# Kernel optimization log

Hardware: AMD Instinct MI355X
Metric: run time of the kernel (lower is better)

Reference implementation:

```python
import jax, jax.numpy as jnp
import numpy as np

N = 50000   # nodes
E = 800000  # edges per relation (avg degree 16)
IN = 128    # input feature dim
H = 2       # attention heads per layer
OUT = 64    # output feats per head
R = 2       # number of relations
NEG_SLOPE = 0.2


def _edge_softmax(e, dst, n):
    # e: [E, H] edge scores; softmax over incoming edges of each dst node
    m = jax.ops.segment_max(e, dst, num_segments=n)  # [N, H]
    m = jnp.where(jnp.isfinite(m), m, 0.0)
    ex = jnp.exp(e - jax.lax.stop_gradient(m)[dst])
    s = jax.ops.segment_sum(ex, dst, num_segments=n)  # [N, H]
    return ex / s[dst]


def _gat_layer(h, W, al, ar, b, src, dst):
    # h: [N, in]; W: [R, in, H*OUT]; al/ar: [R, H, OUT]; b: [R, H*OUT]
    # src/dst: [R, E] int32. HeteroGraphConv with sum aggregation over relations.
    acc = jnp.zeros((N, H, OUT), h.dtype)
    for r in range(R):  # small fixed relation count
        f = (h @ W[r]).reshape(N, H, OUT)           # projected feats
        el = (f * al[r]).sum(-1)                    # [N, H]
        er = (f * ar[r]).sum(-1)                    # [N, H]
        e = jax.nn.leaky_relu(el[src[r]] + er[dst[r]], NEG_SLOPE)  # [E, H]
        a = _edge_softmax(e, dst[r], N)             # [E, H]
        msg = f[src[r]] * a[:, :, None]             # [E, H, OUT]
        agg = jax.ops.segment_sum(msg, dst[r], num_segments=N)     # [N, H, OUT]
        acc = acc + jax.nn.elu(agg + b[r].reshape(1, H, OUT))
    return acc.reshape(N, H * OUT)  # flatten(1)


def setup_inputs() -> dict:
    key = jax.random.key(0)
    k = jax.random.split(key, 13)
    s = 0.05
    f32 = jnp.float32
    return {
        "x": jax.random.normal(k[0], (N, IN), f32),
        "W0": jax.random.normal(k[1], (R, IN, H * OUT), f32) * s,
        "al0": jax.random.normal(k[2], (R, H, OUT), f32) * s,
        "ar0": jax.random.normal(k[3], (R, H, OUT), f32) * s,
        "b0": jax.random.normal(k[4], (R, H * OUT), f32) * s,
        "W1": jax.random.normal(k[5], (R, H * OUT, H * OUT), f32) * s,
        "al1": jax.random.normal(k[6], (R, H, OUT), f32) * s,
        "ar1": jax.random.normal(k[7], (R, H, OUT), f32) * s,
        "b1": jax.random.normal(k[8], (R, H * OUT), f32) * s,
        "src0": jax.random.randint(k[9], (R, E), 0, N, jnp.int32),
        "dst0": jax.random.randint(k[10], (R, E), 0, N, jnp.int32),
        "src1": jax.random.randint(k[11], (R, E), 0, N, jnp.int32),
        "dst1": jax.random.randint(k[12], (R, E), 0, N, jnp.int32),
    }


def reference(x, W0, al0, ar0, b0, W1, al1, ar1, b1, src0, dst0, src1, dst1):
    h = _gat_layer(x, W0, al0, ar0, b0, src0, dst0)  # [N, H*OUT]
    h = _gat_layer(h, W1, al1, ar1, b1, src1, dst1)  # [N, H*OUT]
    return h
```

## Files before the change

### kernel.cpp

```cpp
#include <hip/hip_runtime.h>

#define NN 50000
#define NE 800000
#define DIM 128
#define NB 128
#define CH 4096
#define CAP 8192
#define MAXDEG 64
#define BPSET ((NE + CH - 1) / CH)
#define NBIN_BLOCKS (4 * BPSET)

typedef unsigned int uint;
typedef unsigned short ushort;
typedef __attribute__((ext_vector_type(8))) short v8s;
typedef __attribute__((ext_vector_type(4))) float v4f;

__device__ __forceinline__ ushort f2bf(float f) {
    union { float f; uint i; } c; c.f = f;
    const uint r = (c.i + 0x7fffu + ((c.i >> 16) & 1u)) >> 16;
    return (ushort)r;
}

__device__ __forceinline__ void conv_body(
    const float* __restrict__ W0, const float* __restrict__ W1,
    ushort* __restrict__ WT, int bid)
{
    const int t = bid * 256 + threadIdx.x;
#pragma unroll
    for (int i = 0; i < 4; i++) {
        const int o = t * 4 + i;
        const int m = o >> 14, rem = o & 16383;
        const int nrow = rem >> 7, k = rem & 127;
        const float* src = (m < 2) ? (W0 + (size_t)m * 16384)
                                   : (W1 + (size_t)(m - 2) * 16384);
        WT[o] = f2bf(src[k * 128 + nrow]);
    }
}

__device__ __forceinline__ void gemm_body(
    ushort (*tile)[136],
    const ushort* __restrict__ hbf, const float* __restrict__ xf,
    const ushort* __restrict__ WT,
    const float* __restrict__ al, const float* __restrict__ ar,
    ushort* __restrict__ fg0, ushort* __restrict__ fg1,
    float* __restrict__ elb, int n, int is_f32, int bid)
{
    const int tid = threadIdx.x;
    const int w = tid >> 6, lane = tid & 63;
    const int quad = lane >> 4, l16 = lane & 15;
    const int row0 = bid * 64 + w * 16;

    int arow = row0 + l16;
    if (arow >= n) arow = n - 1;

    v8s afr[4];
    if (is_f32) {
        const float* ap = xf + (size_t)arow * DIM + quad * 8;
#pragma unroll
        for (int kt = 0; kt < 4; kt++) {
            const float4 a0 = *(const float4*)(ap + kt * 32);
            const float4 a1 = *(const float4*)(ap + kt * 32 + 4);
            ushort tmp[8] = { f2bf(a0.x), f2bf(a0.y), f2bf(a0.z), f2bf(a0.w),
                              f2bf(a1.x), f2bf(a1.y), f2bf(a1.z), f2bf(a1.w) };
            afr[kt] = *(const v8s*)tmp;
        }
    } else {
        const ushort* ap = hbf + (size_t)arow * DIM + quad * 8;
#pragma unroll
        for (int kt = 0; kt < 4; kt++) afr[kt] = *(const v8s*)(ap + kt * 32);
    }

    for (int rel = 0; rel < 2; rel++) {
        const ushort* bp = WT + (size_t)rel * DIM * DIM + (size_t)l16 * DIM + quad * 8;
        v4f acc[8];
#pragma unroll
        for (int nt = 0; nt < 8; nt++) acc[nt] = (v4f)0.0f;
#pragma unroll
        for (int kt = 0; kt < 4; kt++) {
#pragma unroll
            for (int nt = 0; nt < 8; nt++) {
                const v8s b = *(const v8s*)(bp + (size_t)nt * 16 * DIM + kt * 32);
                acc[nt] = __builtin_amdgcn_mfma_f32_16x16x32_bf16(afr[kt], b, acc[nt], 0, 0, 0);
            }
        }

        const float* alr = al + rel * DIM;
        const float* arr = ar + rel * DIM;
        float pel[4][2], per2[4][2];
#pragma unroll
        for (int r = 0; r < 4; r++)
            pel[r][0] = pel[r][1] = per2[r][0] = per2[r][1] = 0.f;
#pragma unroll
        for (int nt = 0; nt < 8; nt++) {
            const int col = nt * 16 + l16;
            const float av = alr[col], rv = arr[col];
            const int head = nt >> 2;
#pragma unroll
            for (int r = 0; r < 4; r++) {
                pel[r][head] += acc[nt][r] * av;
                per2[r][head] += acc[nt][r] * rv;
            }
        }
#pragma unroll
        for (int o = 1; o < 16; o <<= 1) {
#pragma unroll
            for (int r = 0; r < 4; r++) {
#pragma unroll
                for (int h = 0; h < 2; h++) {
                    pel[r][h] += __shfl_xor(pel[r][h], o);
                    per2[r][h] += __shfl_xor(per2[r][h], o);
                }
            }
        }
        float* elp = elb + (size_t)rel * NN * 4;
        float* erp = elp + (size_t)NN * 2;
        if (l16 == 0) {
#pragma unroll
            for (int r = 0; r < 4; r++) {
                const int row = row0 + quad * 4 + r;
                if (row < n) {
#pragma unroll
                    for (int h = 0; h < 2; h++) {
                        elp[row * 2 + h] = pel[r][h];
                        erp[row * 2 + h] = per2[r][h];
                    }
                }
            }
        }

        __syncthreads();
        const int lr0 = w * 16 + quad * 4;
#pragma unroll
        for (int nt = 0; nt < 8; nt++) {
            const int col = nt * 16 + l16;
#pragma unroll
            for (int r = 0; r < 4; r++)
                tile[lr0 + r][col] = f2bf(acc[nt][r]);
        }
        __syncthreads();
        ushort* fgr = rel ? fg1 : fg0;
        const int srow = tid >> 2, ch = tid & 3;
        const int grow = bid * 64 + srow;
        if (grow < n) {
            const uint4* lp = (const uint4*)&tile[srow][ch * 32];
            uint4* gp = (uint4*)(fgr + (size_t)grow * DIM + ch * 32);
            gp[0] = lp[0];
            gp[1] = lp[1];
            gp[2] = lp[2];
            gp[3] = lp[3];
        }
    }
}

__global__ __launch_bounds__(256) void gemm_dual(
    const ushort* __restrict__ hbf, const float* __restrict__ xf,
    const ushort* __restrict__ WT,
    const float* __restrict__ al, const float* __restrict__ ar,
    ushort* __restrict__ fg0, ushort* __restrict__ fg1,
    float* __restrict__ elb, int n, int is_f32)
{
    __shared__ ushort tile[64][136];
    gemm_body(tile, hbf, xf, WT, al, ar, fg0, fg1, elb, n, is_f32, blockIdx.x);
}

__device__ __forceinline__ void bin_body(
    char* smem,
    const int* __restrict__ dst0, const int* __restrict__ dst1,
    const int* __restrict__ src0, const int* __restrict__ src1,
    int* __restrict__ gcur, uint* __restrict__ binned, int bid)
{
    int* hist  = (int*)smem;
    int* ebase = hist + NB;
    int* lcur  = ebase + NB;
    int* gbase = lcur + NB;
    int* sc    = gbase + NB;
    uint* stage = (uint*)(sc + NB);

    const int s = bid / BPSET, cb = bid - s * BPSET;
    const int* dstp = (s < 2) ? (dst0 + (size_t)s * NE) : (dst1 + (size_t)(s - 2) * NE);
    const int* srcp = (s < 2) ? (src0 + (size_t)s * NE) : (src1 + (size_t)(s - 2) * NE);
    const int e0 = cb * CH;
    const int t = threadIdx.x;

    if (t < NB) hist[t] = 0;
    __syncthreads();

    int myd[16], mys[16];
#pragma unroll
    for (int k = 0; k < 16; k++) {
        const int e = e0 + t + k * 256;
        if (e < NE) {
            const int d = dstp[e];
            myd[k] = d;
            mys[k] = srcp[e];
            atomicAdd(&hist[(d * NB) / NN], 1);
        } else myd[k] = -1;
    }
    __syncthreads();
    if (t < NB) sc[t] = hist[t];
    __syncthreads();
    for (int o = 1; o < NB; o <<= 1) {
        int tv = 0;
        if (t < NB && t >= o) tv = sc[t - o];
        __syncthreads();
        if (t < NB) sc[t] += tv;
        __syncthreads();
    }
    if (t < NB) {
        ebase[t] = sc[t] - hist[t];
        lcur[t]  = sc[t] - hist[t];
        gbase[t] = (s * NB + t) * CAP + atomicAdd(&gcur[s * NB + t], hist[t]);
    }
    __syncthreads();
#pragma unroll
    for (int k = 0; k < 16; k++) {
        if (myd[k] >= 0) {
            const int b = (myd[k] * NB) / NN;
            const int p = atomicAdd(&lcur[b], 1);
            stage[p] = ((uint)myd[k] << 16) | (uint)mys[k];
        }
    }
    __syncthreads();
    const int total = ebase[NB - 1] + hist[NB - 1];
    for (int i = t; i < total; i += 256) {
        const uint v = stage[i];
        const int b = ((int)(v >> 16) * NB) / NN;
        binned[gbase[b] + (i - ebase[b])] = v;
    }
}

__global__ __launch_bounds__(256) void prep_a(
    const float* __restrict__ W0, const float* __restrict__ W1,
    ushort* __restrict__ WT,
    const int* __restrict__ dst0, const int* __restrict__ dst1,
    const int* __restrict__ src0, const int* __restrict__ src1,
    int* __restrict__ gcur, uint* __restrict__ binned)
{
    __shared__ __align__(16) char smem[18944];
    const int bid = blockIdx.x;
    if (bid < 64) {
        conv_body(W0, W1, WT, bid);
    } else {
        bin_body(smem, dst0, dst1, src0, src1, gcur, binned, bid - 64);
    }
}

__device__ __forceinline__ void slot_body(
    int* lcur, const int* __restrict__ gcur, const uint* __restrict__ binned,
    int* __restrict__ cnt, ushort* __restrict__ slots, int bid)
{
    const int s = bid >> 7, b = bid & (NB - 1);
    const int nb0 = (b * NN + NB - 1) / NB;
    int nb1 = ((b + 1) * NN + NB - 1) / NB;
    if (nb1 > NN) nb1 = NN;
    const int nloc = nb1 - nb0;
    int fill = gcur[s * NB + b];
    if (fill > CAP) fill = CAP;
    const uint* bslot = binned + (size_t)(s * NB + b) * CAP;
    const int t = threadIdx.x;

    for (int i = t; i < nloc; i += 256) lcur[i] = 0;
    __syncthreads();
    ushort* sbase = slots + (size_t)s * NN * MAXDEG;
    for (int j = t; j < fill; j += 256) {
        const uint v = bslot[j];
        const int d = (int)(v >> 16);
        const int p = atomicAdd(&lcur[d - nb0], 1);
        if (p < MAXDEG) sbase[(size_t)d * MAXDEG + p] = (ushort)(v & 0xffffu);
    }
    __syncthreads();
    for (int i = t; i < nloc; i += 256) {
        const int c = lcur[i];
        cnt[s * NN + nb0 + i] = c < MAXDEG ? c : MAXDEG;
    }
}

__global__ __launch_bounds__(256) void prep_b(
    const float* __restrict__ xf, const ushort* __restrict__ WT,
    const float* __restrict__ al, const float* __restrict__ ar,
    ushort* __restrict__ fg0, ushort* __restrict__ fg1,
    float* __restrict__ elb,
    const int* __restrict__ gcur, const uint* __restrict__ binned,
    int* __restrict__ cnt, ushort* __restrict__ slots, int gblocks)
{
    __shared__ __align__(16) char smem[17408];
    const int bid = blockIdx.x;
    if (bid < gblocks) {
        gemm_body((ushort(*)[136])smem, nullptr, xf, WT, al, ar,
                  fg0, fg1, elb, NN, 1, bid);
    } else {
        slot_body((int*)smem, gcur, binned, cnt, slots, bid - gblocks);
    }
}

__device__ __forceinline__ float elu(float v) { return v > 0.f ? v : expm1f(v); }
__device__ __forceinline__ float2 bfpair(uint u) {
    union { uint i; float f; } lo, hi;
    lo.i = u << 16;
    hi.i = u & 0xffff0000u;
    return make_float2(lo.f, hi.f);
}

__global__ __launch_bounds__(256) void aggregate_dual(
    const int* __restrict__ cnt0, const ushort* __restrict__ sl0,
    const int* __restrict__ cnt1, const ushort* __restrict__ sl1,
    const float2* __restrict__ el0, const float2* __restrict__ er0,
    const float2* __restrict__ el1, const float2* __restrict__ er1,
    const ushort* __restrict__ fg0, const ushort* __restrict__ fg1,
    const float* __restrict__ bias0, const float* __restrict__ bias1,
    float* __restrict__ outf, ushort* __restrict__ outbf, int obf)
{
    __shared__ uint soff[4][64];
    __shared__ float wts[4][2][64];
    const int wv = (blockIdx.x * 256 + threadIdx.x) >> 6;
    if (wv >= NN) return;
    const int lane = threadIdx.x & 63;
    const int wid = threadIdx.x >> 6;

    const int* cnts[2] = {cnt0, cnt1};
    const ushort* sls[2] = {sl0, sl1};
    const float2* els[2] = {el0, el1};
    const float2* ers[2] = {er0, er1};
    const ushort* fgs[2] = {fg0, fg1};
    const float* biases[2] = {bias0, bias1};

    float oacc0 = 0.f, oacc1 = 0.f;

#pragma unroll
    for (int rel = 0; rel < 2; rel++) {
        int deg = cnts[rel][wv];
        if (deg > MAXDEG) deg = MAXDEG;
        const float2 erd = ers[rel][wv];
        float2 acc = make_float2(0.f, 0.f);

        uint sof = 0;
        float ex0 = 0.f, ex1 = 0.f;
        if (lane < deg) {
            const int s = sls[rel][(size_t)wv * MAXDEG + lane];
            const float2 e = els[rel][s];
            float e0 = e.x + erd.x, e1 = e.y + erd.y;
            e0 = e0 > 0.f ? e0 : 0.2f * e0;
            e1 = e1 > 0.f ? e1 : 0.2f * e1;
            ex0 = __expf(e0);
            ex1 = __expf(e1);
            sof = (uint)s << 8;
        }
        float den0 = ex0, den1 = ex1;
        for (int o = 32; o > 0; o >>= 1) {
            den0 += __shfl_xor(den0, o);
            den1 += __shfl_xor(den1, o);
        }
        const float inv0 = 1.0f / den0, inv1 = 1.0f / den1;
        soff[wid][lane] = sof;
        wts[wid][0][lane] = ex0 * inv0;
        wts[wid][1][lane] = ex1 * inv1;
        const char* fgb = (const char*)fgs[rel] + lane * 4;
        const float* wrow = wts[wid][lane >> 5];
        const uint* sorow = soff[wid];
        const int dp = (deg + 15) & ~15;
        for (int tt = 0; tt < dp; tt += 16) {
            uint off[16];
            float wgt[16];
#pragma unroll
            for (int k = 0; k < 16; k++) {
                off[k] = sorow[tt + k];
                wgt[k] = wrow[tt + k];
            }
            uint u[16];
#pragma unroll
            for (int k = 0; k < 16; k++)
                u[k] = *(const uint*)(fgb + off[k]);
#pragma unroll
            for (int k = 0; k < 16; k++) {
                const float2 f = bfpair(u[k]);
                acc.x += f.x * wgt[k];
                acc.y += f.y * wgt[k];
            }
        }

        const float b0 = biases[rel][2 * lane], b1 = biases[rel][2 * lane + 1];
        oacc0 += elu(acc.x + b0);
        oacc1 += elu(acc.y + b1);
    }

    if (obf) {
        ushort tmp[2] = { f2bf(oacc0), f2bf(oacc1) };
        *(uint*)(outbf + (size_t)wv * DIM + 2 * lane) = *(const uint*)tmp;
    } else {
        float* op = outf + (size_t)wv * DIM + 2 * lane;
        op[0] = oacc0; op[1] = oacc1;
    }
}

extern "C" void kernel_launch(void* const* d_in, const int* in_sizes, int n_in,
                              void* d_out, int out_size, void* d_ws, size_t ws_size,
                              hipStream_t stream)
{
    const float* x   = (const float*)d_in[0];
    const float* W0  = (const float*)d_in[1];
    const float* al0 = (const float*)d_in[2];
    const float* ar0 = (const float*)d_in[3];
    const float* b0  = (const float*)d_in[4];
    const float* W1  = (const float*)d_in[5];
    const float* al1 = (const float*)d_in[6];
    const float* ar1 = (const float*)d_in[7];
    const float* b1  = (const float*)d_in[8];
    const int* src0 = (const int*)d_in[9];
    const int* dst0 = (const int*)d_in[10];
    const int* src1 = (const int*)d_in[11];
    const int* dst1 = (const int*)d_in[12];
    float* out = (float*)d_out;

    char* w = (char*)d_ws;
    auto alloc = [&](size_t bytes) {
        char* p = w; w += (bytes + 255) & ~(size_t)255; return p;
    };
    ushort* h1bf   = (ushort*)alloc((size_t)NN * DIM * 2);
    ushort* fg0    = (ushort*)alloc((size_t)NN * DIM * 2);
    ushort* fg1    = (ushort*)alloc((size_t)NN * DIM * 2);
    ushort* WT     = (ushort*)alloc((size_t)4 * DIM * DIM * 2);
    float*  elb    = (float*)alloc((size_t)8 * NN * 4);
    int*    cnt    = (int*)alloc((size_t)4 * NN * 4);
    ushort* slots  = (ushort*)alloc((size_t)4 * NN * MAXDEG * 2);
    uint*   binned = (uint*)alloc((size_t)4 * NB * CAP * 4);
    int*    gcur   = (int*)alloc((size_t)4 * NB * 4);

    const int gblocks = (NN + 63) / 64;

    hipMemsetAsync(gcur, 0, (size_t)4 * NB * 4, stream);
    prep_a<<<64 + NBIN_BLOCKS, 256, 0, stream>>>(
        W0, W1, WT, dst0, dst1, src0, src1, gcur, binned);
    prep_b<<<gblocks + 4 * NB, 256, 0, stream>>>(
        x, WT, al0, ar0, fg0, fg1, elb, gcur, binned, cnt, slots, gblocks);

    for (int L = 0; L < 2; L++) {
        if (L) {
            gemm_dual<<<gblocks, 256, 0, stream>>>(
                h1bf, nullptr, WT + (size_t)2 * DIM * DIM, al1, ar1,
                fg0, fg1, elb, NN, 0);
        }
        const float* b = L ? b1 : b0;
        const int es0 = L * 2, es1 = L * 2 + 1;
        float* el0p = elb;
        float* er0p = elb + (size_t)NN * 2;
        float* el1p = elb + (size_t)NN * 4;
        float* er1p = elb + (size_t)NN * 6;
        aggregate_dual<<<(NN * 64 + 255) / 256, 256, 0, stream>>>(
            cnt + (size_t)es0 * NN, slots + (size_t)es0 * NN * MAXDEG,
            cnt + (size_t)es1 * NN, slots + (size_t)es1 * NN * MAXDEG,
            (const float2*)el0p, (const float2*)er0p,
            (const float2*)el1p, (const float2*)er1p,
            fg0, fg1, b, b + DIM,
            L ? out : nullptr, L ? nullptr : h1bf, L ? 0 : 1);
    }
}
```

Before: 346.1 us.

## Stage slot lists in shared memory and split fused prep kernel

The slot-building step now scatters edge sources into a shared-memory window per destination bin and then writes the whole window to global memory with coalesced 16-byte stores. Previously each edge did a scattered 2-byte global write. The layer-0 GEMM is no longer fused with slot building in one launch and now runs as its own gemm_dual launch, which adds a kernel launch. The large shared array (about 50KB) limits occupancy of slot_build. The aggregate kernel also drops its redundant degree clamp.

```diff
diff --git a/kernel.cpp b/kernel.cpp
--- a/kernel.cpp
+++ b/kernel.cpp
@@ -7,6 +7,7 @@
 #define CH 4096
 #define CAP 8192
 #define MAXDEG 64
+#define WINMAX 391
 #define BPSET ((NE + CH - 1) / CH)
 #define NBIN_BLOCKS (4 * BPSET)
 
@@ -37,18 +38,18 @@
     }
 }
 
-__device__ __forceinline__ void gemm_body(
-    ushort (*tile)[136],
+__global__ __launch_bounds__(256) void gemm_dual(
     const ushort* __restrict__ hbf, const float* __restrict__ xf,
     const ushort* __restrict__ WT,
     const float* __restrict__ al, const float* __restrict__ ar,
     ushort* __restrict__ fg0, ushort* __restrict__ fg1,
-    float* __restrict__ elb, int n, int is_f32, int bid)
-{
+    float* __restrict__ elb, int n, int is_f32)
+{
+    __shared__ ushort tile[64][136];
     const int tid = threadIdx.x;
     const int w = tid >> 6, lane = tid & 63;
     const int quad = lane >> 4, l16 = lane & 15;
-    const int row0 = bid * 64 + w * 16;
+    const int row0 = blockIdx.x * 64 + w * 16;
 
     int arow = row0 + l16;
     if (arow >= n) arow = n - 1;
@@ -140,7 +141,7 @@
         __syncthreads();
         ushort* fgr = rel ? fg1 : fg0;
         const int srow = tid >> 2, ch = tid & 3;
-        const int grow = bid * 64 + srow;
+        const int grow = blockIdx.x * 64 + srow;
         if (grow < n) {
             const uint4* lp = (const uint4*)&tile[srow][ch * 32];
             uint4* gp = (uint4*)(fgr + (size_t)grow * DIM + ch * 32);
@@ -150,17 +151,6 @@
             gp[3] = lp[3];
         }
     }
-}
-
-__global__ __launch_bounds__(256) void gemm_dual(
-    const ushort* __restrict__ hbf, const float* __restrict__ xf,
-    const ushort* __restrict__ WT,
-    const float* __restrict__ al, const float* __restrict__ ar,
-    ushort* __restrict__ fg0, ushort* __restrict__ fg1,
-    float* __restrict__ elb, int n, int is_f32)
-{
-    __shared__ ushort tile[64][136];
-    gemm_body(tile, hbf, xf, WT, al, ar, fg0, fg1, elb, n, is_f32, blockIdx.x);
 }
 
 __device__ __forceinline__ void bin_body(
@@ -245,10 +235,13 @@
     }
 }
 
-__device__ __forceinline__ void slot_body(
-    int* lcur, const int* __restrict__ gcur, const uint* __restrict__ binned,
-    int* __restrict__ cnt, ushort* __restrict__ slots, int bid)
-{
+__global__ __launch_bounds__(256) void slot_build(
+    const int* __restrict__ gcur, const uint* __restrict__ binned,
+    int* __restrict__ cnt, ushort* __restrict__ slots)
+{
+    __shared__ ushort win[WINMAX * MAXDEG];
+    __shared__ int lcur[WINMAX];
+    const int bid = blockIdx.x;
     const int s = bid >> 7, b = bid & (NB - 1);
     const int nb0 = (b * NN + NB - 1) / NB;
     int nb1 = ((b + 1) * NN + NB - 1) / NB;
@@ -259,37 +252,24 @@
     const uint* bslot = binned + (size_t)(s * NB + b) * CAP;
     const int t = threadIdx.x;
 
+    uint* wz = (uint*)win;
+    for (int i = t; i < WINMAX * MAXDEG / 2; i += 256) wz[i] = 0;
     for (int i = t; i < nloc; i += 256) lcur[i] = 0;
     __syncthreads();
-    ushort* sbase = slots + (size_t)s * NN * MAXDEG;
     for (int j = t; j < fill; j += 256) {
         const uint v = bslot[j];
-        const int d = (int)(v >> 16);
-        const int p = atomicAdd(&lcur[d - nb0], 1);
-        if (p < MAXDEG) sbase[(size_t)d * MAXDEG + p] = (ushort)(v & 0xffffu);
-    }
-    __syncthreads();
+        const int d = (int)(v >> 16) - nb0;
+        const int p = atomicAdd(&lcur[d], 1);
+        if (p < MAXDEG) win[d * MAXDEG + p] = (ushort)(v & 0xffffu);
+    }
+    __syncthreads();
+    const uint4* wsrc = (const uint4*)win;
+    uint4* wdst = (uint4*)(slots + ((size_t)s * NN + nb0) * MAXDEG);
+    const int nq = nloc * (MAXDEG / 8);
+    for (int i = t; i < nq; i += 256) wdst[i] = wsrc[i];
     for (int i = t; i < nloc; i += 256) {
         const int c = lcur[i];
         cnt[s * NN + nb0 + i] = c < MAXDEG ? c : MAXDEG;
-    }
-}
-
-__global__ __launch_bounds__(256) void prep_b(
-    const float* __restrict__ xf, const ushort* __restrict__ WT,
-    const float* __restrict__ al, const float* __restrict__ ar,
-    ushort* __restrict__ fg0, ushort* __restrict__ fg1,
-    float* __restrict__ elb,
-    const int* __restrict__ gcur, const uint* __restrict__ binned,
-    int* __restrict__ cnt, ushort* __restrict__ slots, int gblocks)
-{
-    __shared__ __align__(16) char smem[17408];
-    const int bid = blockIdx.x;
-    if (bid < gblocks) {
-        gemm_body((ushort(*)[136])smem, nullptr, xf, WT, al, ar,
-                  fg0, fg1, elb, NN, 1, bid);
-    } else {
-        slot_body((int*)smem, gcur, binned, cnt, slots, bid - gblocks);
     }
 }
 
@@ -328,8 +308,7 @@
 
 #pragma unroll
     for (int rel = 0; rel < 2; rel++) {
-        int deg = cnts[rel][wv];
-        if (deg > MAXDEG) deg = MAXDEG;
+        const int deg = cnts[rel][wv];
         const float2 erd = ers[rel][wv];
         float2 acc = make_float2(0.f, 0.f);
 
@@ -426,26 +405,26 @@
     int*    gcur   = (int*)alloc((size_t)4 * NB * 4);
 
     const int gblocks = (NN + 63) / 64;
+    const int ablocks = (NN * 64 + 255) / 256;
 
     hipMemsetAsync(gcur, 0, (size_t)4 * NB * 4, stream);
     prep_a<<<64 + NBIN_BLOCKS, 256, 0, stream>>>(
         W0, W1, WT, dst0, dst1, src0, src1, gcur, binned);
-    prep_b<<<gblocks + 4 * NB, 256, 0, stream>>>(
-        x, WT, al0, ar0, fg0, fg1, elb, gcur, binned, cnt, slots, gblocks);
+    slot_build<<<4 * NB, 256, 0, stream>>>(gcur, binned, cnt, slots);
 
     for (int L = 0; L < 2; L++) {
-        if (L) {
-            gemm_dual<<<gblocks, 256, 0, stream>>>(
-                h1bf, nullptr, WT + (size_t)2 * DIM * DIM, al1, ar1,
-                fg0, fg1, elb, NN, 0);
-        }
+        gemm_dual<<<gblocks, 256, 0, stream>>>(
+            L ? h1bf : nullptr, L ? nullptr : x,
+            WT + (size_t)L * 2 * DIM * DIM,
+            L ? al1 : al0, L ? ar1 : ar0,
+            fg0, fg1, elb, NN, L ? 0 : 1);
         const float* b = L ? b1 : b0;
         const int es0 = L * 2, es1 = L * 2 + 1;
         float* el0p = elb;
         float* er0p = elb + (size_t)NN * 2;
         float* el1p = elb + (size_t)NN * 4;
         float* er1p = elb + (size_t)NN * 6;
-        aggregate_dual<<<(NN * 64 + 255) / 256, 256, 0, stream>>>(
+        aggregate_dual<<<ablocks, 256, 0, stream>>>(
             cnt + (size_t)es0 * NN, slots + (size_t)es0 * NN * MAXDEG,
             cnt + (size_t)es1 * NN, slots + (size_t)es1 * NN * MAXDEG,
             (const float2*)el0p, (const float2*)er0p,
```

Result: no change. 349.2 us (+0.9%).
